# Kernel tuning notes

Hardware: AMD Instinct MI355X
Metric: run time of the kernel (lower is better)

Reference implementation:

```python
import jax, jax.numpy as jnp
import numpy as np

N_NODES = 100000
N_EDGES = 1600000
N_GRAPHS = 1000
NODES_PER_GRAPH = N_NODES // N_GRAPHS
IN_DIM, HID_DIM, OUT_DIM = 32, 64, 32


def setup_inputs() -> dict:
    key = jax.random.key(0)
    k_x, k_src, k_dst, k_w1, k_w2 = jax.random.split(key, 5)
    x = jax.random.normal(k_x, (N_NODES, IN_DIM), dtype=jnp.float32)
    src = jax.random.randint(k_src, (N_EDGES,), 0, N_NODES, dtype=jnp.int32)
    dst = jax.random.randint(k_dst, (N_EDGES,), 0, N_NODES, dtype=jnp.int32)
    edge_index = jnp.stack([src, dst], axis=0)
    batch = (jnp.arange(N_NODES, dtype=jnp.int32) // NODES_PER_GRAPH)
    W1 = jax.random.normal(k_w1, (IN_DIM, HID_DIM), dtype=jnp.float32) / np.sqrt(IN_DIM)
    b1 = jnp.zeros((HID_DIM,), dtype=jnp.float32)
    W2 = jax.random.normal(k_w2, (HID_DIM, OUT_DIM), dtype=jnp.float32) / np.sqrt(HID_DIM)
    b2 = jnp.zeros((OUT_DIM,), dtype=jnp.float32)
    return {"x": x, "edge_index": edge_index, "batch": batch,
            "W1": W1, "b1": b1, "W2": W2, "b2": b2}


def _gcn_conv(x, W, b, src, dst, deg_inv_sqrt):
    # PyG GCNConv: out = D^{-1/2}(A+I)D^{-1/2} X W + b, deg includes self-loops
    h = x @ W  # [N, F]
    norm = deg_inv_sqrt[src] * deg_inv_sqrt[dst]  # [E]
    agg = jax.ops.segment_sum(h[src] * norm[:, None], dst, num_segments=N_NODES)
    # self-loop contribution: norm = deg^{-1/2} * deg^{-1/2} = 1/deg
    agg = agg + h * (deg_inv_sqrt * deg_inv_sqrt)[:, None]
    return agg + b


def reference(x, edge_index, batch, W1, b1, W2, b2):
    src, dst = edge_index[0], edge_index[1]
    # degree at target nodes, with self-loops
    deg = 1.0 + jax.ops.segment_sum(jnp.ones_like(dst, dtype=x.dtype), dst,
                                    num_segments=N_NODES)
    deg_inv_sqrt = jax.lax.rsqrt(deg)
    h = jax.nn.relu(_gcn_conv(x, W1, b1, src, dst, deg_inv_sqrt))
    h = _gcn_conv(h, W2, b2, src, dst, deg_inv_sqrt)
    # per-graph mean pooling (fused segment mean)
    sums = jax.ops.segment_sum(h, batch, num_segments=N_GRAPHS)
    counts = jax.ops.segment_sum(jnp.ones((h.shape[0],), dtype=h.dtype), batch,
                                 num_segments=N_GRAPHS)
    return sums / counts[:, None]
```

## Files before the change

### kernel.cpp

```cpp
#include <hip/hip_runtime.h>

#define IN_DIM 32
#define HID_DIM 64
#define OUT_DIM 32

#define MAXBUCK 1024
#define CAP 2560
#define EPB 8192

typedef unsigned int u32;
typedef unsigned short u16;
typedef unsigned long long u64;
typedef __attribute__((ext_vector_type(8))) short bf16x8;
typedef __attribute__((ext_vector_type(4))) float f32x4;

static __device__ __forceinline__ u32 bf16rne(float f) {
    u32 u = __float_as_uint(f);
    return (u + 0x7FFFu + ((u >> 16) & 1u)) >> 16;
}
static __device__ __forceinline__ float blo(u32 u) { return __uint_as_float(u << 16); }
static __device__ __forceinline__ float bhi(u32 u) { return __uint_as_float(u & 0xFFFF0000u); }

__global__ __launch_bounds__(1024) void k_bin(const int* __restrict__ src,
                                              const int* __restrict__ dst,
                                              int* __restrict__ cursor,
                                              int* __restrict__ binned,
                                              int E, int nbuck, int npg, u32 M) {
    __shared__ int lcnt[MAXBUCK];
    __shared__ int lbase[MAXBUCK];
    int t = threadIdx.x;
    if (t < MAXBUCK) lcnt[t] = 0;
    __syncthreads();
    int base = blockIdx.x * EPB;
    int dreg[8], breg[8];
#pragma unroll
    for (int k = 0; k < 8; k++) {
        int e = base + k * 1024 + t;
        dreg[k] = (e < E) ? dst[e] : -1;
    }
#pragma unroll
    for (int k = 0; k < 8; k++) {
        if (dreg[k] >= 0) {
            breg[k] = (int)(((u64)(u32)dreg[k] * M) >> 38);
            atomicAdd(&lcnt[breg[k]], 1);
        }
    }
    __syncthreads();
    if (t < nbuck) {
        int c = lcnt[t];
        if (c) lbase[t] = atomicAdd(&cursor[t], c);
        lcnt[t] = 0;
    }
    __syncthreads();
#pragma unroll
    for (int k = 0; k < 8; k++) {
        if (dreg[k] >= 0) {
            int bk = breg[k];
            int dl = dreg[k] - bk * npg;
            int loc = lbase[bk] + atomicAdd(&lcnt[bk], 1);
            if (loc < CAP)
                binned[bk * CAP + loc] = (dl << 17) | src[base + k * 1024 + t];
        }
    }
}

__global__ __launch_bounds__(256) void k_csr(const int* __restrict__ binned,
                                             const int* __restrict__ cursor,
                                             const float* __restrict__ x,
                                             int2* __restrict__ row,
                                             float* __restrict__ dis,
                                             u16* __restrict__ g,
                                             int* __restrict__ meta,
                                             int N, int npg) {
    __shared__ int sEdge[CAP];
    __shared__ int sH[4][128];
    __shared__ int sExcl[128];
    __shared__ int sCur[128];
    __shared__ float sdis[128];
    __shared__ int wsum[2];
    int b = blockIdx.x;
    int t = threadIdx.x;
    int wid = t >> 6;
    int s0 = b * CAP;
    int cnt = cursor[b];
    if (cnt > CAP) cnt = CAP;

    for (int k = t; k < 4 * 128; k += 256) ((int*)sH)[k] = 0;
    __syncthreads();

    for (int k = t; k < cnt; k += 256) {
        int p = binned[s0 + k];
        sEdge[k] = p;
        atomicAdd(&sH[wid][p >> 17], 1);
    }
    __syncthreads();

    if (t < 128) {
        int myv = sH[0][t] + sH[1][t] + sH[2][t] + sH[3][t];
        int lane = t & 63;
        int incl = myv;
#pragma unroll
        for (int o = 1; o < 64; o <<= 1) {
            int up = __shfl_up(incl, o);
            if (lane >= o) incl += up;
        }
        if (lane == 63) wsum[t >> 6] = incl;
        sExcl[t] = incl - myv;
        sCur[t] = 0;
        sH[0][t] = myv;
    }
    __syncthreads();
    if (t < 128) {
        int exclv = sExcl[t] + ((t >= 64) ? wsum[0] : 0);
        sExcl[t] = exclv;
        int myv = sH[0][t];
        float d = rsqrtf(1.0f + (float)myv);
        sdis[t] = d;
        int node = b * npg + t;
        if (t < npg && node < N) {
            row[node] = make_int2(s0 + exclv, s0 + exclv + myv);
            dis[node] = d;
        }
    }
    __syncthreads();

    for (int k = t; k < cnt; k += 256) {
        int p = sEdge[k];
        int dl = p >> 17;
        int pos = sExcl[dl] + atomicAdd(&sCur[dl], 1);
        meta[s0 + pos] = p & 0x1FFFF;
    }

    int nbLo = b * npg;
    int nn = N - nbLo;
    if (nn > npg) nn = npg;
    if (nn < 0) nn = 0;
    int halfE = nn * 16;
    const float* xb = x + (size_t)nbLo * 32;
    u32* gb = (u32*)(g + (size_t)nbLo * 32);
    for (int j = t; j < halfE; j += 256) {
        int e0 = j * 2;
        float dd = sdis[e0 >> 5];
        gb[j] = bf16rne(dd * xb[e0]) | (bf16rne(dd * xb[e0 + 1]) << 16);
    }
}

__global__ __launch_bounds__(256) void k_agg(const u16* __restrict__ g,
                                             const int* __restrict__ meta,
                                             const int2* __restrict__ row,
                                             const float* __restrict__ dis,
                                             u16* __restrict__ outf, int N) {
    int gid = blockIdx.x * 256 + threadIdx.x;
    int i = gid >> 5;
    if (i >= N) return;
    int l = threadIdx.x & 31;
    int grp = (l >> 2) & 7;
    int sub = l & 3;
    const uint4* gv = (const uint4*)g;

    float a0 = 0.f, a1 = 0.f, a2 = 0.f, a3 = 0.f;
    float a4 = 0.f, a5 = 0.f, a6 = 0.f, a7 = 0.f;
    int2 rw = row[i];
    int e = rw.x, end = rw.y;
    for (; e + 16 <= end; e += 16) {
        int s0 = meta[e + grp];
        int s1 = meta[e + 8 + grp];
        uint4 v0 = gv[s0 * 4 + sub];
        uint4 v1 = gv[s1 * 4 + sub];
        a0 += blo(v0.x); a1 += bhi(v0.x); a2 += blo(v0.y); a3 += bhi(v0.y);
        a4 += blo(v0.z); a5 += bhi(v0.z); a6 += blo(v0.w); a7 += bhi(v0.w);
        a0 += blo(v1.x); a1 += bhi(v1.x); a2 += blo(v1.y); a3 += bhi(v1.y);
        a4 += blo(v1.z); a5 += bhi(v1.z); a6 += blo(v1.w); a7 += bhi(v1.w);
    }
    if (e + grp < end) {
        uint4 v = gv[meta[e + grp] * 4 + sub];
        a0 += blo(v.x); a1 += bhi(v.x); a2 += blo(v.y); a3 += bhi(v.y);
        a4 += blo(v.z); a5 += bhi(v.z); a6 += blo(v.w); a7 += bhi(v.w);
    }
    if (e + 8 + grp < end) {
        uint4 v = gv[meta[e + 8 + grp] * 4 + sub];
        a0 += blo(v.x); a1 += bhi(v.x); a2 += blo(v.y); a3 += bhi(v.y);
        a4 += blo(v.z); a5 += bhi(v.z); a6 += blo(v.w); a7 += bhi(v.w);
    }
#pragma unroll
    for (int m = 4; m <= 16; m <<= 1) {
        a0 += __shfl_xor(a0, m); a1 += __shfl_xor(a1, m);
        a2 += __shfl_xor(a2, m); a3 += __shfl_xor(a3, m);
        a4 += __shfl_xor(a4, m); a5 += __shfl_xor(a5, m);
        a6 += __shfl_xor(a6, m); a7 += __shfl_xor(a7, m);
    }
    if (grp == 0) {
        uint4 sv = gv[i * 4 + sub];
        float d = dis[i];
        u32 o0 = bf16rne(d * (a0 + blo(sv.x))) | (bf16rne(d * (a1 + bhi(sv.x))) << 16);
        u32 o1 = bf16rne(d * (a2 + blo(sv.y))) | (bf16rne(d * (a3 + bhi(sv.y))) << 16);
        u32 o2 = bf16rne(d * (a4 + blo(sv.z))) | (bf16rne(d * (a5 + bhi(sv.z))) << 16);
        u32 o3 = bf16rne(d * (a6 + blo(sv.w))) | (bf16rne(d * (a7 + bhi(sv.w))) << 16);
        ((uint4*)outf)[i * 4 + sub] = make_uint4(o0, o1, o2, o3);
    }
}

__global__ __launch_bounds__(256) void k_mlp(const u16* __restrict__ aggX,
                                             const float* __restrict__ W1,
                                             const float* __restrict__ b1,
                                             const float* __restrict__ W2,
                                             const float* __restrict__ dis,
                                             u16* __restrict__ t2, int N) {
    __shared__ float sHls[4][16 * 65];
    int t = threadIdx.x;
    int w = t >> 6;
    int L = t & 63;
    int q = L >> 4;
    int col = L & 15;
    int base = blockIdx.x * 64 + w * 16;

    int arow = base + col;
    uint4 av = (arow < N) ? ((const uint4*)aggX)[(size_t)arow * 4 + q]
                          : make_uint4(0, 0, 0, 0);
    bf16x8 afrag = *(bf16x8*)&av;

    bf16x8 b1f[4];
#pragma unroll
    for (int nt = 0; nt < 4; nt++) {
#pragma unroll
        for (int jj = 0; jj < 8; jj++)
            b1f[nt][jj] = (short)bf16rne(W1[(q * 8 + jj) * HID_DIM + nt * 16 + col]);
    }
    bf16x8 b2f[2][2];
#pragma unroll
    for (int ks = 0; ks < 2; ks++)
#pragma unroll
        for (int nt = 0; nt < 2; nt++) {
#pragma unroll
            for (int jj = 0; jj < 8; jj++)
                b2f[ks][nt][jj] =
                    (short)bf16rne(W2[(ks * 32 + q * 8 + jj) * OUT_DIM + nt * 16 + col]);
        }

#pragma unroll
    for (int nt = 0; nt < 4; nt++) {
        float bias = b1[nt * 16 + col];
        f32x4 c = {bias, bias, bias, bias};
        c = __builtin_amdgcn_mfma_f32_16x16x32_bf16(afrag, b1f[nt], c, 0, 0, 0);
#pragma unroll
        for (int r = 0; r < 4; r++)
            sHls[w][(q * 4 + r) * 65 + nt * 16 + col] = fmaxf(c[r], 0.0f);
    }
    __syncthreads();

    bf16x8 a2[2];
#pragma unroll
    for (int ks = 0; ks < 2; ks++) {
#pragma unroll
        for (int jj = 0; jj < 8; jj++)
            a2[ks][jj] = (short)bf16rne(sHls[w][col * 65 + ks * 32 + q * 8 + jj]);
    }

    f32x4 C2[2];
#pragma unroll
    for (int nt = 0; nt < 2; nt++) {
        f32x4 c = {0.f, 0.f, 0.f, 0.f};
        c = __builtin_amdgcn_mfma_f32_16x16x32_bf16(a2[0], b2f[0][nt], c, 0, 0, 0);
        c = __builtin_amdgcn_mfma_f32_16x16x32_bf16(a2[1], b2f[1][nt], c, 0, 0, 0);
        C2[nt] = c;
    }

#pragma unroll
    for (int r = 0; r < 4; r++) {
        int node = base + q * 4 + r;
        if (node < N) {
            float dd = dis[node];
            t2[(size_t)node * 32 + col]      = (u16)bf16rne(dd * C2[0][r]);
            t2[(size_t)node * 32 + 16 + col] = (u16)bf16rne(dd * C2[1][r]);
        }
    }
}

__global__ __launch_bounds__(512) void k_pool2(const int* __restrict__ binned,
                                               const int* __restrict__ cursor,
                                               const u16* __restrict__ gB,
                                               const float* __restrict__ dis,
                                               const float* __restrict__ b2,
                                               float* __restrict__ out,
                                               int N, int npg, float inv_npg) {
    __shared__ float sdis[128];
    __shared__ float sacc[32];
    int b = blockIdx.x;
    int t = threadIdx.x;
    if (t < 128) {
        int node = b * npg + t;
        sdis[t] = (t < npg && node < N) ? dis[node] : 0.0f;
    }
    if (t < 32) sacc[t] = 0.0f;
    __syncthreads();

    int s0 = b * CAP;
    int cnt = cursor[b];
    if (cnt > CAP) cnt = CAP;
    int sub = t & 3;
    int et = t >> 2;
    const uint4* gv = (const uint4*)gB;

    float a0 = 0.f, a1 = 0.f, a2 = 0.f, a3 = 0.f;
    float a4 = 0.f, a5 = 0.f, a6 = 0.f, a7 = 0.f;
#pragma unroll 4
    for (int e = et; e < cnt; e += 128) {
        int p = binned[s0 + e];
        uint4 v = gv[(u32)(p & 0x1FFFF) * 4 + sub];
        float w = sdis[p >> 17];
        a0 = fmaf(w, blo(v.x), a0); a1 = fmaf(w, bhi(v.x), a1);
        a2 = fmaf(w, blo(v.y), a2); a3 = fmaf(w, bhi(v.y), a3);
        a4 = fmaf(w, blo(v.z), a4); a5 = fmaf(w, bhi(v.z), a5);
        a6 = fmaf(w, blo(v.w), a6); a7 = fmaf(w, bhi(v.w), a7);
    }
#pragma unroll
    for (int m = 4; m <= 32; m <<= 1) {
        a0 += __shfl_xor(a0, m); a1 += __shfl_xor(a1, m);
        a2 += __shfl_xor(a2, m); a3 += __shfl_xor(a3, m);
        a4 += __shfl_xor(a4, m); a5 += __shfl_xor(a5, m);
        a6 += __shfl_xor(a6, m); a7 += __shfl_xor(a7, m);
    }
    if ((t & 63) < 4) {
        atomicAdd(&sacc[sub * 8 + 0], a0);
        atomicAdd(&sacc[sub * 8 + 1], a1);
        atomicAdd(&sacc[sub * 8 + 2], a2);
        atomicAdd(&sacc[sub * 8 + 3], a3);
        atomicAdd(&sacc[sub * 8 + 4], a4);
        atomicAdd(&sacc[sub * 8 + 5], a5);
        atomicAdd(&sacc[sub * 8 + 6], a6);
        atomicAdd(&sacc[sub * 8 + 7], a7);
    }

    float accs = 0.0f;
    int elems = npg * 32;
    const u16* gbase = gB + (size_t)b * npg * 32;
    int nbLo = b * npg;
    for (int k = t; k < elems; k += 512) {
        int node = k >> 5;
        if (nbLo + node < N)
            accs = fmaf(sdis[node], __uint_as_float((u32)gbase[k] << 16), accs);
    }
    atomicAdd(&sacc[t & 31], accs);
    __syncthreads();

    if (t < 32)
        out[b * 32 + t] = fmaf(sacc[t], inv_npg, b2[t]);
}

extern "C" void kernel_launch(void* const* d_in, const int* in_sizes, int n_in,
                              void* d_out, int out_size, void* d_ws, size_t ws_size,
                              hipStream_t stream) {
    const float* x   = (const float*)d_in[0];
    const int* eidx  = (const int*)d_in[1];
    const float* W1  = (const float*)d_in[3];
    const float* b1  = (const float*)d_in[4];
    const float* W2  = (const float*)d_in[5];
    const float* b2  = (const float*)d_in[6];
    float* out       = (float*)d_out;

    const int N = in_sizes[0] / IN_DIM;
    const int E = in_sizes[1] / 2;
    const int G = out_size / OUT_DIM;
    const int npg = N / G;
    const int nbuck = G;
    const int* src = eidx;
    const int* dst = eidx + E;
    const u32 M = (u32)(((1ull << 38) + npg - 1) / (u64)npg);

    char* ws = (char*)d_ws;
    size_t off = 0;
    auto alloc = [&](size_t bytes) -> char* {
        char* p = ws + off;
        off = (off + bytes + 255) & ~(size_t)255;
        return p;
    };
    int*   cursor = (int*)alloc(MAXBUCK * sizeof(int));
    int2*  row    = (int2*)alloc((size_t)N * sizeof(int2));
    float* dis    = (float*)alloc((size_t)N * sizeof(float));
    int*   binned = (int*)alloc((size_t)nbuck * CAP * sizeof(int));
    int*   meta   = (int*)alloc((size_t)nbuck * CAP * sizeof(int));
    u16*   g      = (u16*)alloc((size_t)N * IN_DIM * sizeof(u16));
    u16*   bufA   = (u16*)alloc((size_t)N * IN_DIM * sizeof(u16));
    u16*   bufB   = (u16*)alloc((size_t)N * OUT_DIM * sizeof(u16));
    (void)ws_size;

    hipMemsetAsync(cursor, 0, MAXBUCK * sizeof(int), stream);

    k_bin<<<(E + EPB - 1) / EPB, 1024, 0, stream>>>(src, dst, cursor, binned,
                                                    E, nbuck, npg, M);
    k_csr<<<nbuck, 256, 0, stream>>>(binned, cursor, x, row, dis, g, meta, N, npg);
    k_agg<<<((size_t)N * 32 + 255) / 256, 256, 0, stream>>>(g, meta, row, dis, bufA, N);
    k_mlp<<<(N + 63) / 64, 256, 0, stream>>>(bufA, W1, b1, W2, dis, bufB, N);
    k_pool2<<<nbuck, 512, 0, stream>>>(binned, cursor, bufB, dis, b2, out,
                                       N, npg, 1.0f / (float)npg);
}
```

Before: 159.4 us.

## Replace bucketed binning and CSR build with atomic-slot ELL neighbor lists

The two-pass edge binning (per-block LDS histograms into 1000 buckets, then a per-bucket CSR sort) is replaced by a single scatter kernel. Each edge atomically claims a slot in its destination's fixed 48-entry neighbor row, and a separate elementwise kernel computes degree normalization and the scaled bf16 features. Aggregation and pooling now index the padded ELL rows directly. This removes a kernel and the LDS sort, but adds one global atomic per edge and random scattered writes. Pooling also has to scan padded slots, and any node with more than 48 in-edges would lose edges.

```diff
diff --git a/kernel.cpp b/kernel.cpp
--- a/kernel.cpp
+++ b/kernel.cpp
@@ -4,9 +4,7 @@
 #define HID_DIM 64
 #define OUT_DIM 32
 
-#define MAXBUCK 1024
-#define CAP 2560
-#define EPB 8192
+#define NCAP 48
 
 typedef unsigned int u32;
 typedef unsigned short u16;
@@ -21,133 +19,36 @@
 static __device__ __forceinline__ float blo(u32 u) { return __uint_as_float(u << 16); }
 static __device__ __forceinline__ float bhi(u32 u) { return __uint_as_float(u & 0xFFFF0000u); }
 
-__global__ __launch_bounds__(1024) void k_bin(const int* __restrict__ src,
+__global__ __launch_bounds__(256) void k_scat(const int* __restrict__ src,
                                               const int* __restrict__ dst,
-                                              int* __restrict__ cursor,
-                                              int* __restrict__ binned,
-                                              int E, int nbuck, int npg, u32 M) {
-    __shared__ int lcnt[MAXBUCK];
-    __shared__ int lbase[MAXBUCK];
-    int t = threadIdx.x;
-    if (t < MAXBUCK) lcnt[t] = 0;
-    __syncthreads();
-    int base = blockIdx.x * EPB;
-    int dreg[8], breg[8];
-#pragma unroll
-    for (int k = 0; k < 8; k++) {
-        int e = base + k * 1024 + t;
-        dreg[k] = (e < E) ? dst[e] : -1;
-    }
-#pragma unroll
-    for (int k = 0; k < 8; k++) {
-        if (dreg[k] >= 0) {
-            breg[k] = (int)(((u64)(u32)dreg[k] * M) >> 38);
-            atomicAdd(&lcnt[breg[k]], 1);
-        }
-    }
-    __syncthreads();
-    if (t < nbuck) {
-        int c = lcnt[t];
-        if (c) lbase[t] = atomicAdd(&cursor[t], c);
-        lcnt[t] = 0;
-    }
-    __syncthreads();
-#pragma unroll
-    for (int k = 0; k < 8; k++) {
-        if (dreg[k] >= 0) {
-            int bk = breg[k];
-            int dl = dreg[k] - bk * npg;
-            int loc = lbase[bk] + atomicAdd(&lcnt[bk], 1);
-            if (loc < CAP)
-                binned[bk * CAP + loc] = (dl << 17) | src[base + k * 1024 + t];
-        }
-    }
-}
-
-__global__ __launch_bounds__(256) void k_csr(const int* __restrict__ binned,
-                                             const int* __restrict__ cursor,
+                                              int* __restrict__ degc,
+                                              int* __restrict__ nbr,
+                                              int E) {
+    int e = blockIdx.x * 256 + threadIdx.x;
+    if (e >= E) return;
+    int d = dst[e];
+    int slot = atomicAdd(&degc[d], 1);
+    if (slot < NCAP)
+        nbr[(size_t)d * NCAP + slot] = src[e];
+}
+
+__global__ __launch_bounds__(256) void k_pre(const int* __restrict__ degc,
                                              const float* __restrict__ x,
-                                             int2* __restrict__ row,
                                              float* __restrict__ dis,
                                              u16* __restrict__ g,
-                                             int* __restrict__ meta,
-                                             int N, int npg) {
-    __shared__ int sEdge[CAP];
-    __shared__ int sH[4][128];
-    __shared__ int sExcl[128];
-    __shared__ int sCur[128];
-    __shared__ float sdis[128];
-    __shared__ int wsum[2];
-    int b = blockIdx.x;
-    int t = threadIdx.x;
-    int wid = t >> 6;
-    int s0 = b * CAP;
-    int cnt = cursor[b];
-    if (cnt > CAP) cnt = CAP;
-
-    for (int k = t; k < 4 * 128; k += 256) ((int*)sH)[k] = 0;
-    __syncthreads();
-
-    for (int k = t; k < cnt; k += 256) {
-        int p = binned[s0 + k];
-        sEdge[k] = p;
-        atomicAdd(&sH[wid][p >> 17], 1);
-    }
-    __syncthreads();
-
-    if (t < 128) {
-        int myv = sH[0][t] + sH[1][t] + sH[2][t] + sH[3][t];
-        int lane = t & 63;
-        int incl = myv;
-#pragma unroll
-        for (int o = 1; o < 64; o <<= 1) {
-            int up = __shfl_up(incl, o);
-            if (lane >= o) incl += up;
-        }
-        if (lane == 63) wsum[t >> 6] = incl;
-        sExcl[t] = incl - myv;
-        sCur[t] = 0;
-        sH[0][t] = myv;
-    }
-    __syncthreads();
-    if (t < 128) {
-        int exclv = sExcl[t] + ((t >= 64) ? wsum[0] : 0);
-        sExcl[t] = exclv;
-        int myv = sH[0][t];
-        float d = rsqrtf(1.0f + (float)myv);
-        sdis[t] = d;
-        int node = b * npg + t;
-        if (t < npg && node < N) {
-            row[node] = make_int2(s0 + exclv, s0 + exclv + myv);
-            dis[node] = d;
-        }
-    }
-    __syncthreads();
-
-    for (int k = t; k < cnt; k += 256) {
-        int p = sEdge[k];
-        int dl = p >> 17;
-        int pos = sExcl[dl] + atomicAdd(&sCur[dl], 1);
-        meta[s0 + pos] = p & 0x1FFFF;
-    }
-
-    int nbLo = b * npg;
-    int nn = N - nbLo;
-    if (nn > npg) nn = npg;
-    if (nn < 0) nn = 0;
-    int halfE = nn * 16;
-    const float* xb = x + (size_t)nbLo * 32;
-    u32* gb = (u32*)(g + (size_t)nbLo * 32);
-    for (int j = t; j < halfE; j += 256) {
-        int e0 = j * 2;
-        float dd = sdis[e0 >> 5];
-        gb[j] = bf16rne(dd * xb[e0]) | (bf16rne(dd * xb[e0 + 1]) << 16);
-    }
+                                             int N) {
+    int j = blockIdx.x * 256 + threadIdx.x;
+    if (j >= N * 16) return;
+    int node = j >> 4;
+    float dd = rsqrtf(1.0f + (float)degc[node]);
+    if ((j & 15) == 0) dis[node] = dd;
+    const float* xb = x + (size_t)node * 32 + (j & 15) * 2;
+    ((u32*)g)[j] = bf16rne(dd * xb[0]) | (bf16rne(dd * xb[1]) << 16);
 }
 
 __global__ __launch_bounds__(256) void k_agg(const u16* __restrict__ g,
-                                             const int* __restrict__ meta,
-                                             const int2* __restrict__ row,
+                                             const int* __restrict__ nbr,
+                                             const int* __restrict__ degc,
                                              const float* __restrict__ dis,
                                              u16* __restrict__ outf, int N) {
     int gid = blockIdx.x * 256 + threadIdx.x;
@@ -160,11 +61,12 @@
 
     float a0 = 0.f, a1 = 0.f, a2 = 0.f, a3 = 0.f;
     float a4 = 0.f, a5 = 0.f, a6 = 0.f, a7 = 0.f;
-    int2 rw = row[i];
-    int e = rw.x, end = rw.y;
+    int deg = degc[i];
+    if (deg > NCAP) deg = NCAP;
+    int e = i * NCAP, end = i * NCAP + deg;
     for (; e + 16 <= end; e += 16) {
-        int s0 = meta[e + grp];
-        int s1 = meta[e + 8 + grp];
+        int s0 = nbr[e + grp];
+        int s1 = nbr[e + 8 + grp];
         uint4 v0 = gv[s0 * 4 + sub];
         uint4 v1 = gv[s1 * 4 + sub];
         a0 += blo(v0.x); a1 += bhi(v0.x); a2 += blo(v0.y); a3 += bhi(v0.y);
@@ -173,12 +75,12 @@
         a4 += blo(v1.z); a5 += bhi(v1.z); a6 += blo(v1.w); a7 += bhi(v1.w);
     }
     if (e + grp < end) {
-        uint4 v = gv[meta[e + grp] * 4 + sub];
+        uint4 v = gv[nbr[e + grp] * 4 + sub];
         a0 += blo(v.x); a1 += bhi(v.x); a2 += blo(v.y); a3 += bhi(v.y);
         a4 += blo(v.z); a5 += bhi(v.z); a6 += blo(v.w); a7 += bhi(v.w);
     }
     if (e + 8 + grp < end) {
-        uint4 v = gv[meta[e + 8 + grp] * 4 + sub];
+        uint4 v = gv[nbr[e + 8 + grp] * 4 + sub];
         a0 += blo(v.x); a1 += bhi(v.x); a2 += blo(v.y); a3 += bhi(v.y);
         a4 += blo(v.z); a5 += bhi(v.z); a6 += blo(v.w); a7 += bhi(v.w);
     }
@@ -276,42 +178,48 @@
     }
 }
 
-__global__ __launch_bounds__(512) void k_pool2(const int* __restrict__ binned,
-                                               const int* __restrict__ cursor,
+__global__ __launch_bounds__(512) void k_pool2(const int* __restrict__ nbr,
+                                               const int* __restrict__ degc,
                                                const u16* __restrict__ gB,
                                                const float* __restrict__ dis,
                                                const float* __restrict__ b2,
                                                float* __restrict__ out,
                                                int N, int npg, float inv_npg) {
     __shared__ float sdis[128];
+    __shared__ int sdeg[128];
     __shared__ float sacc[32];
     int b = blockIdx.x;
     int t = threadIdx.x;
     if (t < 128) {
         int node = b * npg + t;
-        sdis[t] = (t < npg && node < N) ? dis[node] : 0.0f;
+        bool v = (t < npg && node < N);
+        sdis[t] = v ? dis[node] : 0.0f;
+        int dg = v ? degc[node] : 0;
+        sdeg[t] = dg > NCAP ? NCAP : dg;
     }
     if (t < 32) sacc[t] = 0.0f;
     __syncthreads();
 
-    int s0 = b * CAP;
-    int cnt = cursor[b];
-    if (cnt > CAP) cnt = CAP;
     int sub = t & 3;
     int et = t >> 2;
     const uint4* gv = (const uint4*)gB;
+    const int* nb = nbr + (size_t)b * npg * NCAP;
 
     float a0 = 0.f, a1 = 0.f, a2 = 0.f, a3 = 0.f;
     float a4 = 0.f, a5 = 0.f, a6 = 0.f, a7 = 0.f;
-#pragma unroll 4
-    for (int e = et; e < cnt; e += 128) {
-        int p = binned[s0 + e];
-        uint4 v = gv[(u32)(p & 0x1FFFF) * 4 + sub];
-        float w = sdis[p >> 17];
-        a0 = fmaf(w, blo(v.x), a0); a1 = fmaf(w, bhi(v.x), a1);
-        a2 = fmaf(w, blo(v.y), a2); a3 = fmaf(w, bhi(v.y), a3);
-        a4 = fmaf(w, blo(v.z), a4); a5 = fmaf(w, bhi(v.z), a5);
-        a6 = fmaf(w, blo(v.w), a6); a7 = fmaf(w, bhi(v.w), a7);
+    int total = npg * NCAP;
+    for (int gs = et; gs < total; gs += 128) {
+        int n = gs / NCAP;
+        int s = gs - n * NCAP;
+        if (s < sdeg[n]) {
+            int srcv = nb[gs];
+            uint4 v = gv[(u32)srcv * 4 + sub];
+            float w = sdis[n];
+            a0 = fmaf(w, blo(v.x), a0); a1 = fmaf(w, bhi(v.x), a1);
+            a2 = fmaf(w, blo(v.y), a2); a3 = fmaf(w, bhi(v.y), a3);
+            a4 = fmaf(w, blo(v.z), a4); a5 = fmaf(w, bhi(v.z), a5);
+            a6 = fmaf(w, blo(v.w), a6); a7 = fmaf(w, bhi(v.w), a7);
+        }
     }
 #pragma unroll
     for (int m = 4; m <= 32; m <<= 1) {
@@ -362,10 +270,8 @@
     const int E = in_sizes[1] / 2;
     const int G = out_size / OUT_DIM;
     const int npg = N / G;
-    const int nbuck = G;
     const int* src = eidx;
     const int* dst = eidx + E;
-    const u32 M = (u32)(((1ull << 38) + npg - 1) / (u64)npg);
 
     char* ws = (char*)d_ws;
     size_t off = 0;
@@ -374,23 +280,20 @@
         off = (off + bytes + 255) & ~(size_t)255;
         return p;
     };
-    int*   cursor = (int*)alloc(MAXBUCK * sizeof(int));
-    int2*  row    = (int2*)alloc((size_t)N * sizeof(int2));
-    float* dis    = (float*)alloc((size_t)N * sizeof(float));
-    int*   binned = (int*)alloc((size_t)nbuck * CAP * sizeof(int));
-    int*   meta   = (int*)alloc((size_t)nbuck * CAP * sizeof(int));
-    u16*   g      = (u16*)alloc((size_t)N * IN_DIM * sizeof(u16));
-    u16*   bufA   = (u16*)alloc((size_t)N * IN_DIM * sizeof(u16));
-    u16*   bufB   = (u16*)alloc((size_t)N * OUT_DIM * sizeof(u16));
+    int*   degc = (int*)alloc((size_t)N * sizeof(int));
+    float* dis  = (float*)alloc((size_t)N * sizeof(float));
+    int*   nbr  = (int*)alloc((size_t)N * NCAP * sizeof(int));
+    u16*   g    = (u16*)alloc((size_t)N * IN_DIM * sizeof(u16));
+    u16*   bufA = (u16*)alloc((size_t)N * IN_DIM * sizeof(u16));
+    u16*   bufB = (u16*)alloc((size_t)N * OUT_DIM * sizeof(u16));
     (void)ws_size;
 
-    hipMemsetAsync(cursor, 0, MAXBUCK * sizeof(int), stream);
-
-    k_bin<<<(E + EPB - 1) / EPB, 1024, 0, stream>>>(src, dst, cursor, binned,
-                                                    E, nbuck, npg, M);
-    k_csr<<<nbuck, 256, 0, stream>>>(binned, cursor, x, row, dis, g, meta, N, npg);
-    k_agg<<<((size_t)N * 32 + 255) / 256, 256, 0, stream>>>(g, meta, row, dis, bufA, N);
+    hipMemsetAsync(degc, 0, (size_t)N * sizeof(int), stream);
+
+    k_scat<<<(E + 255) / 256, 256, 0, stream>>>(src, dst, degc, nbr, E);
+    k_pre<<<((size_t)N * 16 + 255) / 256, 256, 0, stream>>>(degc, x, dis, g, N);
+    k_agg<<<((size_t)N * 32 + 255) / 256, 256, 0, stream>>>(g, nbr, degc, dis, bufA, N);
     k_mlp<<<(N + 63) / 64, 256, 0, stream>>>(bufA, W1, b1, W2, dis, bufB, N);
-    k_pool2<<<nbuck, 512, 0, stream>>>(binned, cursor, bufB, dis, b2, out,
-                                       N, npg, 1.0f / (float)npg);
-}
+    k_pool2<<<G, 512, 0, stream>>>(nbr, degc, bufB, dis, b2, out,
+                                   N, npg, 1.0f / (float)npg);
+}
```

Result: slower. 264.9 us (+66.2%).
